# Kernel optimization log

Hardware: AMD Instinct MI355X
Metric: run time of the kernel (lower is better)

Reference implementation:

```python
import jax, jax.numpy as jnp
import numpy as np

BATCH, S, N_DIM, B_SIZE = 512, 66, 304, 128

def setup_inputs() -> dict:
    key = jax.random.key(0)
    kx, kw = jax.random.split(key)
    x = jax.random.normal(kx, (BATCH, S, N_DIM), dtype=jnp.float32)
    W = jax.random.normal(kw, (B_SIZE, N_DIM), dtype=jnp.float32) * (1.0 / np.sqrt(N_DIM))
    b = jnp.zeros((B_SIZE,), dtype=jnp.float32)
    return {"x": x, "W": W, "b": b}

def reference(x, W, b):
    # Linear projection into tree space: (batch, S, B_size)
    t = jnp.einsum('bsd,kd->bsk', x, W) + b
    # Pairwise squared distances over sentence positions, same math as
    # expand/transpose/subtract/pow(2)/sum in the torch module.
    diff = t[:, :, None, :] - t[:, None, :, :]        # (batch, S, S, B_size)
    return jnp.sum(diff * diff, axis=-1)               # (batch, S, S)
```

## Files before the change

### kernel.cpp

```cpp
#include <hip/hip_runtime.h>
#include <hip/hip_bf16.h>

#define NBATCH 512
#define NS 66
#define ND 304
#define NK 128

#define XROWS 80
#define XSTRIDE_B 640
#define XBYTES (XROWS * XSTRIDE_B)
#define TSTRIDE_B 256
#define TBYTES (XROWS * TSTRIDE_B)
#define GSTRIDE 84

typedef __attribute__((ext_vector_type(8))) short bf16x8;
typedef __attribute__((ext_vector_type(4))) short s16x4;
typedef __attribute__((ext_vector_type(4))) float f32x4;

__device__ __forceinline__ short f2bf(float x) {
    return __builtin_bit_cast(short, __float2bfloat16(x));
}

__global__ __launch_bounds__(256, 2) void treeprobe_mfma(
    const float* __restrict__ x,
    const float* __restrict__ W,
    float* __restrict__ out)
{
    __shared__ __align__(16) char lds[XBYTES + TBYTES];
    char* const t_lds = lds + XBYTES;
    float* const G = (float*)lds;

    const int tid   = threadIdx.x;
    const int batch = blockIdx.x;
    const int lane  = tid & 63;
    const int wv    = tid >> 6;
    const int lr    = lane & 15;
    const int lg    = lane >> 4;

    bf16x8 wfrag[2][10];
#pragma unroll
    for (int nt = 0; nt < 2; ++nt) {
        const int c = (wv * 2 + nt) * 16 + lr;
        const float* __restrict__ wr = W + c * ND;
#pragma unroll
        for (int kk = 0; kk < 10; ++kk) {
            const int k0 = kk * 32 + lg * 8;
            bf16x8 f = {0, 0, 0, 0, 0, 0, 0, 0};
            if (k0 < ND) {
                const float4 p0 = *reinterpret_cast<const float4*>(wr + k0);
                const float4 p1 = *reinterpret_cast<const float4*>(wr + k0 + 4);
                f[0] = f2bf(p0.x); f[1] = f2bf(p0.y);
                f[2] = f2bf(p0.z); f[3] = f2bf(p0.w);
                f[4] = f2bf(p1.x); f[5] = f2bf(p1.y);
                f[6] = f2bf(p1.z); f[7] = f2bf(p1.w);
            }
            wfrag[nt][kk] = f;
        }
    }

    for (int i = tid; i < XBYTES / 16; i += 256) {
        *reinterpret_cast<f32x4*>(lds + i * 16) = (f32x4){0.f, 0.f, 0.f, 0.f};
    }
    __syncthreads();

    const float* __restrict__ xb = x + (size_t)batch * NS * ND;
    for (int e = tid; e < NS * ND / 4; e += 256) {
        const int s  = e / 76;
        const int d4 = (e % 76) * 4;
        const float4 v = *reinterpret_cast<const float4*>(xb + e * 4);
        int byte = s * XSTRIDE_B + d4 * 2;
        byte ^= (s & 7) << 4;
        s16x4 sv;
        sv[0] = f2bf(v.x); sv[1] = f2bf(v.y);
        sv[2] = f2bf(v.z); sv[3] = f2bf(v.w);
        *reinterpret_cast<s16x4*>(lds + byte) = sv;
    }
    __syncthreads();

    f32x4 acc[5][2];
#pragma unroll
    for (int mt = 0; mt < 5; ++mt)
#pragma unroll
        for (int nt = 0; nt < 2; ++nt)
            acc[mt][nt] = (f32x4){0.f, 0.f, 0.f, 0.f};

#pragma unroll
    for (int kk = 0; kk < 10; ++kk) {
        bf16x8 a[5];
#pragma unroll
        for (int mt = 0; mt < 5; ++mt) {
            const int row = mt * 16 + lr;
            int byte = row * XSTRIDE_B + kk * 64 + lg * 16;
            byte ^= (row & 7) << 4;
            a[mt] = *reinterpret_cast<const bf16x8*>(lds + byte);
        }
#pragma unroll
        for (int mt = 0; mt < 5; ++mt)
#pragma unroll
            for (int nt = 0; nt < 2; ++nt)
                acc[mt][nt] = __builtin_amdgcn_mfma_f32_16x16x32_bf16(
                    a[mt], wfrag[nt][kk], acc[mt][nt], 0, 0, 0);
    }

#pragma unroll
    for (int mt = 0; mt < 5; ++mt)
#pragma unroll
        for (int nt = 0; nt < 2; ++nt) {
            const int col = (wv * 2 + nt) * 16 + lr;
#pragma unroll
            for (int r = 0; r < 4; ++r) {
                const int row = mt * 16 + lg * 4 + r;
                int byte = row * TSTRIDE_B + col * 2;
                byte ^= (row & 7) << 4;
                *reinterpret_cast<short*>(t_lds + byte) = f2bf(acc[mt][nt][r]);
            }
        }
    __syncthreads();

    for (int tile = wv; tile < 25; tile += 4) {
        const int ti = tile / 5, tj = tile % 5;
        f32x4 g = (f32x4){0.f, 0.f, 0.f, 0.f};
#pragma unroll
        for (int kk = 0; kk < 4; ++kk) {
            const int ra = ti * 16 + lr;
            int ba = ra * TSTRIDE_B + kk * 64 + lg * 16;
            ba ^= (ra & 7) << 4;
            const int rb = tj * 16 + lr;
            int bb = rb * TSTRIDE_B + kk * 64 + lg * 16;
            bb ^= (rb & 7) << 4;
            const bf16x8 av = *reinterpret_cast<const bf16x8*>(t_lds + ba);
            const bf16x8 bv = *reinterpret_cast<const bf16x8*>(t_lds + bb);
            g = __builtin_amdgcn_mfma_f32_16x16x32_bf16(av, bv, g, 0, 0, 0);
        }
#pragma unroll
        for (int r = 0; r < 4; ++r) {
            const int row = ti * 16 + lg * 4 + r;
            const int col = tj * 16 + lr;
            G[row * GSTRIDE + col] = g[r];
        }
    }
    __syncthreads();

    float* __restrict__ ob = out + (size_t)batch * NS * NS;
    for (int e = tid; e < NS * NS / 2; e += 256) {
        const int i = e / 33;
        const int j = (e % 33) * 2;
        const float nii = G[i * GSTRIDE + i];
        float2 r;
        r.x = nii + G[j * GSTRIDE + j] - 2.f * G[i * GSTRIDE + j];
        r.y = nii + G[(j + 1) * GSTRIDE + (j + 1)] - 2.f * G[i * GSTRIDE + j + 1];
        *reinterpret_cast<float2*>(ob + i * NS + j) = r;
    }
}

extern "C" void kernel_launch(void* const* d_in, const int* in_sizes, int n_in,
                              void* d_out, int out_size, void* d_ws, size_t ws_size,
                              hipStream_t stream) {
    const float* x = (const float*)d_in[0];
    const float* W = (const float*)d_in[1];
    float* out = (float*)d_out;

    treeprobe_mfma<<<NBATCH, 256, 0, stream>>>(x, W, out);
}
```

Baseline: 23.88 us.

## Double block size to 512 threads with one N-tile per wave

Raises the block from 4 to 8 waves, so each wave computes one 16-column slice of the projection instead of two. Per-wave W fragment registers and accumulators are halved, and the staging, Gram-tile and output loops are spread over more threads. This adds memory-level parallelism and latency hiding within a block. In exchange, each A fragment read from LDS now feeds only one MFMA, which doubles LDS read traffic for the x tile, and the launch-bounds occupancy request rises to 4 blocks.

```diff
diff --git a/kernel.cpp b/kernel.cpp
--- a/kernel.cpp
+++ b/kernel.cpp
@@ -13,6 +13,8 @@
 #define TBYTES (XROWS * TSTRIDE_B)
 #define GSTRIDE 84
 
+#define NTHREADS 512
+
 typedef __attribute__((ext_vector_type(8))) short bf16x8;
 typedef __attribute__((ext_vector_type(4))) short s16x4;
 typedef __attribute__((ext_vector_type(4))) float f32x4;
@@ -21,7 +23,7 @@
     return __builtin_bit_cast(short, __float2bfloat16(x));
 }
 
-__global__ __launch_bounds__(256, 2) void treeprobe_mfma(
+__global__ __launch_bounds__(NTHREADS, 4) void treeprobe_mfma(
     const float* __restrict__ x,
     const float* __restrict__ W,
     float* __restrict__ out)
@@ -37,10 +39,9 @@
     const int lr    = lane & 15;
     const int lg    = lane >> 4;
 
-    bf16x8 wfrag[2][10];
-#pragma unroll
-    for (int nt = 0; nt < 2; ++nt) {
-        const int c = (wv * 2 + nt) * 16 + lr;
+    bf16x8 wfrag[10];
+    {
+        const int c = wv * 16 + lr;
         const float* __restrict__ wr = W + c * ND;
 #pragma unroll
         for (int kk = 0; kk < 10; ++kk) {
@@ -54,17 +55,17 @@
                 f[4] = f2bf(p1.x); f[5] = f2bf(p1.y);
                 f[6] = f2bf(p1.z); f[7] = f2bf(p1.w);
             }
-            wfrag[nt][kk] = f;
+            wfrag[kk] = f;
         }
     }
 
-    for (int i = tid; i < XBYTES / 16; i += 256) {
+    for (int i = tid; i < XBYTES / 16; i += NTHREADS) {
         *reinterpret_cast<f32x4*>(lds + i * 16) = (f32x4){0.f, 0.f, 0.f, 0.f};
     }
     __syncthreads();
 
     const float* __restrict__ xb = x + (size_t)batch * NS * ND;
-    for (int e = tid; e < NS * ND / 4; e += 256) {
+    for (int e = tid; e < NS * ND / 4; e += NTHREADS) {
         const int s  = e / 76;
         const int d4 = (e % 76) * 4;
         const float4 v = *reinterpret_cast<const float4*>(xb + e * 4);
@@ -77,12 +78,9 @@
     }
     __syncthreads();
 
-    f32x4 acc[5][2];
+    f32x4 acc[5];
 #pragma unroll
-    for (int mt = 0; mt < 5; ++mt)
-#pragma unroll
-        for (int nt = 0; nt < 2; ++nt)
-            acc[mt][nt] = (f32x4){0.f, 0.f, 0.f, 0.f};
+    for (int mt = 0; mt < 5; ++mt) acc[mt] = (f32x4){0.f, 0.f, 0.f, 0.f};
 
 #pragma unroll
     for (int kk = 0; kk < 10; ++kk) {
@@ -96,28 +94,26 @@
         }
 #pragma unroll
         for (int mt = 0; mt < 5; ++mt)
-#pragma unroll
-            for (int nt = 0; nt < 2; ++nt)
-                acc[mt][nt] = __builtin_amdgcn_mfma_f32_16x16x32_bf16(
-                    a[mt], wfrag[nt][kk], acc[mt][nt], 0, 0, 0);
+            acc[mt] = __builtin_amdgcn_mfma_f32_16x16x32_bf16(
+                a[mt], wfrag[kk], acc[mt], 0, 0, 0);
     }
 
+    {
+        const int col = wv * 16 + lr;
 #pragma unroll
-    for (int mt = 0; mt < 5; ++mt)
-#pragma unroll
-        for (int nt = 0; nt < 2; ++nt) {
-            const int col = (wv * 2 + nt) * 16 + lr;
+        for (int mt = 0; mt < 5; ++mt) {
 #pragma unroll
             for (int r = 0; r < 4; ++r) {
                 const int row = mt * 16 + lg * 4 + r;
                 int byte = row * TSTRIDE_B + col * 2;
                 byte ^= (row & 7) << 4;
-                *reinterpret_cast<short*>(t_lds + byte) = f2bf(acc[mt][nt][r]);
+                *reinterpret_cast<short*>(t_lds + byte) = f2bf(acc[mt][r]);
             }
         }
+    }
     __syncthreads();
 
-    for (int tile = wv; tile < 25; tile += 4) {
+    for (int tile = wv; tile < 25; tile += 8) {
         const int ti = tile / 5, tj = tile % 5;
         f32x4 g = (f32x4){0.f, 0.f, 0.f, 0.f};
 #pragma unroll
@@ -142,7 +138,7 @@
     __syncthreads();
 
     float* __restrict__ ob = out + (size_t)batch * NS * NS;
-    for (int e = tid; e < NS * NS / 2; e += 256) {
+    for (int e = tid; e < NS * NS / 2; e += NTHREADS) {
         const int i = e / 33;
         const int j = (e % 33) * 2;
         const float nii = G[i * GSTRIDE + i];
@@ -160,5 +156,5 @@
     const float* W = (const float*)d_in[1];
     float* out = (float*)d_out;
 
-    treeprobe_mfma<<<NBATCH, 256, 0, stream>>>(x, W, out);
+    treeprobe_mfma<<<NBATCH, NTHREADS, 0, stream>>>(x, W, out);
 }
```

Result: faster. 21.26 us (-11.0%).
